# Kernel tuning notes

Hardware: AMD Instinct MI355X
Metric: run time of the kernel (lower is better)

Reference implementation:

```python
import jax, jax.numpy as jnp
import numpy as np


def setup_inputs() -> dict:
    key = jax.random.key(0)
    k1, k2, k3 = jax.random.split(key, 3)
    B, Cin, Cout, K, H, W = 4, 64, 64, 3, 160, 160
    inputs = jax.random.normal(k1, (B, Cin, H, W), dtype=jnp.float32)
    # fractional dilation rates in [1, 3]
    rate_map = 1.0 + 2.0 * jax.random.uniform(k2, (B, 1, H, W), dtype=jnp.float32)
    # xavier-uniform-ish init
    limit = float(np.sqrt(6.0 / (Cin * K * K + Cout * K * K)))
    weight = jax.random.uniform(k3, (Cout, Cin, K, K), dtype=jnp.float32,
                                minval=-limit, maxval=limit)
    bias = jnp.zeros((Cout,), dtype=jnp.float32)
    return {"inputs": inputs, "weight": weight, "rate_map": rate_map,
            "bias": bias, "stride_h": 1, "stride_w": 1}


def _pdconv2d(inputs, weight, rate_map, bias, stride_h, stride_w):
    """Perspective (fractional, per-pixel) dilated conv with same padding.

    For each output pixel, the KxK taps are placed at center + offset*rate,
    where rate comes from rate_map and may be fractional -> bilinear sampling
    with zeros outside the image.
    """
    B, C, H, W = inputs.shape
    O, _, K, _ = weight.shape
    HO = (H + stride_h - 1) // stride_h
    WO = (W + stride_w - 1) // stride_w

    rate = rate_map[:, 0, ::stride_h, ::stride_w]  # [B,HO,WO]
    cy = (jnp.arange(HO) * stride_h).astype(jnp.float32)
    cx = (jnp.arange(WO) * stride_w).astype(jnp.float32)
    off = jnp.arange(K, dtype=jnp.float32) - (K - 1) / 2.0  # centered taps

    # sampling coords [B,HO,WO,K,K]
    sy = cy[None, :, None, None, None] + off[None, None, None, :, None] * rate[:, :, :, None, None]
    sx = cx[None, None, :, None, None] + off[None, None, None, None, :] * rate[:, :, :, None, None]
    sy = jnp.broadcast_to(sy, (B, HO, WO, K, K))
    sx = jnpp = jnp.broadcast_to(sx, (B, HO, WO, K, K))
    sx = jnp_p = sx  # no-op alias (keeps names clear)

    y0 = jnp.floor(sy)
    x0 = jnp.floor(sx)
    wy = sy - y0  # bilinear weights
    wx = sx - x0
    y0i = y0.astype(jnp.int32)
    x0i = x0.astype(jnp.int32)

    img = inputs.reshape(B, C, H * W)

    def gather(idx):  # idx [B,HO,WO,K,K] -> [B,C,HO,WO,K,K]
        return jax.vmap(lambda im, ix: jnp.take(im, ix, axis=-1))(img, idx)

    acc = jnp.zeros((B, C, HO, WO, K, K), dtype=inputs.dtype)
    corners = [(0, 0, (1 - wy) * (1 - wx)), (0, 1, (1 - wy) * wx),
               (1, 0, wy * (1 - wx)), (1, 1, wy * wx)]
    for dy, dx, cw in corners:
        yy = y0i + dy
        xx = x0i + dx
        valid = (yy >= 0) & (yy < H) & (xx >= 0) & (xx < W)
        idx = jnp.clip(yy, 0, H - 1) * W + jnp.clip(xx, 0, W - 1)
        w = (cw * valid.astype(inputs.dtype))[:, None]  # [B,1,HO,WO,K,K]
        acc = acc + gather(idx) * w

    # [B,C,HO,WO,K,K] x [O,C,K,K] -> [B,O,HO,WO]
    out = jnp.einsum('bchwkl,ockl->bohw', acc, weight)
    return out + bias[None, :, None, None]


def reference(inputs, weight, rate_map, bias, stride_h, stride_w):
    return _pdconv2d(inputs, weight, rate_map, bias, stride_h, stride_w)
```

## Files before the change

kernel.cpp:

```cpp
#include <hip/hip_runtime.h>
#include <hip/hip_bf16.h>

#define NB   4
#define CIN  64
#define COUT 64
#define HH   160
#define WW   160
#define HW   (HH * WW)

#define RT   9
#define CT   39
#define RS   72
#define HIN_SHORTS (RT * CT * RS)

typedef __attribute__((ext_vector_type(8))) short bf16x8;
typedef __attribute__((ext_vector_type(4))) float f32x4;
typedef __attribute__((ext_vector_type(2))) float f32x2;
typedef __attribute__((ext_vector_type(4))) unsigned int u32x4;

static __device__ __forceinline__ short f2bf(float v) {
    return __builtin_bit_cast(short, __float2bfloat16(v));
}

__global__ void wtf_kernel(const float* __restrict__ w, short* __restrict__ wtf) {
    int i = blockIdx.x * 256 + threadIdx.x;
    if (i < 36864) {
        const int j  = i & 7;
        const int l  = (i >> 3) & 63;
        const int mt = (i >> 9) & 3;
        const int ks = (i >> 11) & 1;
        const int t  = i >> 12;
        const int o  = 16 * mt + (l & 15);
        const int c  = 32 * ks + 8 * (l >> 4) + j;
        wtf[i] = f2bf(w[(o * CIN + c) * 9 + t]);
    }
}

__global__ __launch_bounds__(256) void tin_kernel(const float* __restrict__ in,
                                                  short* __restrict__ tin) {
    const int cpx = gridDim.x >> 3;
    const int wb  = (blockIdx.x & 7) * cpx + (blockIdx.x >> 3);
    const int gid = wb * 256 + threadIdx.x;
    if (gid >= NB * HW) return;
    const int b  = gid / HW;
    const int hw = gid - b * HW;
    const float* src = in + (size_t)b * CIN * HW + hw;
    short* dst = tin + (size_t)gid * CIN;
#pragma unroll
    for (int chunk = 0; chunk < 4; ++chunk) {
        union { u32x4 v; short s[8]; } p0, p1;
#pragma unroll
        for (int cc = 0; cc < 8; ++cc)
            p0.s[cc] = f2bf(src[(size_t)(chunk * 16 + cc) * HW]);
#pragma unroll
        for (int cc = 0; cc < 8; ++cc)
            p1.s[cc] = f2bf(src[(size_t)(chunk * 16 + 8 + cc) * HW]);
        *(u32x4*)(dst + chunk * 16)     = p0.v;
        *(u32x4*)(dst + chunk * 16 + 8) = p1.v;
    }
}

static __device__ __forceinline__ void consume_tap(
    const u32x4 v00, const u32x4 v01, const u32x4 v10, const u32x4 v11,
    const float c00, const float c01, const float c10, const float c11,
    const bf16x8 wf0, const bf16x8 wf1, const bf16x8 wf2, const bf16x8 wf3,
    f32x4 acc[4])
{
    union { bf16x8 v; unsigned u[4]; } pf;
#pragma unroll
    for (int wd = 0; wd < 4; ++wd) {
        f32x2 s;
        {
            const unsigned u0 = v00[wd];
            const f32x2 xv = { __builtin_bit_cast(float, u0 << 16),
                               __builtin_bit_cast(float, u0 & 0xffff0000u) };
            s = c00 * xv;
        }
        {
            const unsigned u0 = v01[wd];
            const f32x2 xv = { __builtin_bit_cast(float, u0 << 16),
                               __builtin_bit_cast(float, u0 & 0xffff0000u) };
            s += c01 * xv;
        }
        {
            const unsigned u0 = v10[wd];
            const f32x2 xv = { __builtin_bit_cast(float, u0 << 16),
                               __builtin_bit_cast(float, u0 & 0xffff0000u) };
            s += c10 * xv;
        }
        {
            const unsigned u0 = v11[wd];
            const f32x2 xv = { __builtin_bit_cast(float, u0 << 16),
                               __builtin_bit_cast(float, u0 & 0xffff0000u) };
            s += c11 * xv;
        }
        unsigned r;
        asm("v_cvt_pk_bf16_f32 %0, %1, %2" : "=v"(r) : "v"(s.x), "v"(s.y));
        pf.u[wd] = r;
    }
    acc[0] = __builtin_amdgcn_mfma_f32_16x16x32_bf16(wf0, pf.v, acc[0], 0, 0, 0);
    acc[1] = __builtin_amdgcn_mfma_f32_16x16x32_bf16(wf1, pf.v, acc[1], 0, 0, 0);
    acc[2] = __builtin_amdgcn_mfma_f32_16x16x32_bf16(wf2, pf.v, acc[2], 0, 0, 0);
    acc[3] = __builtin_amdgcn_mfma_f32_16x16x32_bf16(wf3, pf.v, acc[3], 0, 0, 0);
}

__global__ __launch_bounds__(256, 2) void pdconv_halo_kernel(
    const short* __restrict__ tin,
    const short* __restrict__ wtf,
    const float* __restrict__ rate_map,
    const float* __restrict__ bias,
    float* __restrict__ out)
{
    __shared__ short hin[HIN_SHORTS];

    const int tid  = threadIdx.x;
    const int wave = tid >> 6;
    const int lane = tid & 63;
    const int px   = lane & 15;
    const int g    = lane >> 4;

    const int cpx = gridDim.x >> 3;
    const int bid = (blockIdx.x & 7) * cpx + (blockIdx.x >> 3);

    const int b   = bid / 400;
    const int rem = bid - b * 400;
    const int rr  = rem / 5;
    const int cc  = rem - rr * 5;
    const int oy  = 2 * rr - 3;
    const int ox  = 32 * cc - 3;

    const short* ib = tin + (size_t)b * HW * CIN;
#pragma unroll
    for (int it = 0; it < 11; ++it) {
        const int idx = it * 256 + tid;
        if (idx < RT * CT * 8) {
            const int rec = idx >> 3;
            const int cp  = idx & 7;
            const int ty  = rec / CT;
            const int tx  = rec - ty * CT;
            const int gy  = min(max(oy + ty, 0), HH - 1);
            const int gx  = min(max(ox + tx, 0), WW - 1);
            const u32x4 v = *(const u32x4*)(ib + ((size_t)gy * WW + gx) * CIN + cp * 8);
            *(u32x4*)(hin + rec * RS + cp * 8) = v;
        }
    }
    __syncthreads();

    const int row = 2 * rr + (wave >> 1);
    const int col0 = 32 * cc + 16 * (wave & 1);
    const int x   = col0 + px;
    const float rate = rate_map[b * HW + row * WW + x];
    const float fy = (float)row, fx = (float)x;

    const short* wtb = wtf + lane * 8;

    f32x4 acc[4];
#pragma unroll
    for (int mt = 0; mt < 4; ++mt) acc[mt] = (f32x4){0.f, 0.f, 0.f, 0.f};

#pragma unroll 1
    for (int t = 0; t < 9; ++t) {
        const int ky = t / 3;
        const int kx = t - 3 * ky;

        const float sy  = fy + (float)(ky - 1) * rate;
        const float sx  = fx + (float)(kx - 1) * rate;
        const float y0f = floorf(sy), x0f = floorf(sx);
        const float wy  = sy - y0f,   wx  = sx - x0f;
        const int   y0  = (int)y0f,   x0i = (int)x0f;
        const int   y1  = y0 + 1,     x1  = x0i + 1;

        const float omwy = 1.0f - wy, omwx = 1.0f - wx;
        const float vy0 = (y0 >= 0 && y0 < HH) ? 1.0f : 0.0f;
        const float vy1 = (y1 >= 0 && y1 < HH) ? 1.0f : 0.0f;
        const float vx0 = (x0i >= 0 && x0i < WW) ? 1.0f : 0.0f;
        const float vx1 = (x1 >= 0 && x1 < WW) ? 1.0f : 0.0f;

        const float c00 = omwy * omwx * vy0 * vx0;
        const float c01 = omwy * wx   * vy0 * vx1;
        const float c10 = wy   * omwx * vy1 * vx0;
        const float c11 = wy   * wx   * vy1 * vx1;

        const int rec00 = (y0 - oy) * CT + (x0i - ox);
        const short* h00 = hin + rec00 * RS + 8 * g;

        u32x4 v00[2], v01[2], v10[2], v11[2];
#pragma unroll
        for (int ks = 0; ks < 2; ++ks) {
            const short* hk = h00 + 32 * ks;
            v00[ks] = *(const u32x4*)(hk);
            v01[ks] = *(const u32x4*)(hk + RS);
            v10[ks] = *(const u32x4*)(hk + CT * RS);
            v11[ks] = *(const u32x4*)(hk + (CT + 1) * RS);
        }

#pragma unroll
        for (int ks = 0; ks < 2; ++ks) {
            const short* wb = wtb + (size_t)((t * 2 + ks) * 4) * 512;
            const bf16x8 wf0 = *(const bf16x8*)(wb);
            const bf16x8 wf1 = *(const bf16x8*)(wb + 512);
            const bf16x8 wf2 = *(const bf16x8*)(wb + 1024);
            const bf16x8 wf3 = *(const bf16x8*)(wb + 1536);
            consume_tap(v00[ks], v01[ks], v10[ks], v11[ks],
                        c00, c01, c10, c11, wf0, wf1, wf2, wf3, acc);
        }
    }

    float* op = out + (size_t)b * COUT * HW + row * WW + col0 + px;
#pragma unroll
    for (int mt = 0; mt < 4; ++mt) {
        const f32x4 bv = *(const f32x4*)(bias + 16 * mt + 4 * g);
#pragma unroll
        for (int r = 0; r < 4; ++r) {
            const int o = 16 * mt + 4 * g + r;
            op[(size_t)o * HW] = acc[mt][r] + bv[r];
        }
    }
}

__global__ void wt2_kernel(const float* __restrict__ w, short* __restrict__ wt2) {
    int i = blockIdx.x * 256 + threadIdx.x;
    if (i < 9 * COUT * CIN) {
        int c = i & 63, o = (i >> 6) & 63, t = i >> 12;
        wt2[i] = f2bf(w[(o * CIN + c) * 9 + t]);
    }
}

__global__ __launch_bounds__(256) void pdconv_mfma_kernel(
    const float* __restrict__ in, const short* __restrict__ wt2,
    const float* __restrict__ rate_map, const float* __restrict__ bias,
    float* __restrict__ out)
{
    const int tid = threadIdx.x, wave = tid >> 6, lane = tid & 63;
    const int px = lane & 15, g = lane >> 4;
    const int cpx = gridDim.x >> 3;
    const int bid = (blockIdx.x & 7) * cpx + (blockIdx.x >> 3);
    const int base = bid * 64 + wave * 16;
    const int b = base / HW, pix0 = base - b * HW;
    const int y = pix0 / WW, x0 = pix0 - y * WW, x = x0 + px;
    const float rate = rate_map[base + px];
    const float fy = (float)y, fx = (float)x;
    f32x4 acc[4];
#pragma unroll
    for (int mt = 0; mt < 4; ++mt) acc[mt] = (f32x4){0.f, 0.f, 0.f, 0.f};
    const float* img  = in + (size_t)b * CIN * HW;
    const float* imgg = img + (size_t)g * 8 * HW;
#pragma unroll 1
    for (int t = 0; t < 9; ++t) {
        const int ky = t / 3, kx = t - 3 * ky;
        const float sy = fy + (float)(ky - 1) * rate;
        const float sx = fx + (float)(kx - 1) * rate;
        const float y0f = floorf(sy), x0f = floorf(sx);
        const float wy = sy - y0f, wx = sx - x0f;
        const int y0 = (int)y0f, x0i = (int)x0f, y1 = y0 + 1, x1 = x0i + 1;
        const float omwy = 1.0f - wy, omwx = 1.0f - wx;
        const float vy0 = (y0 >= 0 && y0 < HH) ? 1.0f : 0.0f;
        const float vy1 = (y1 >= 0 && y1 < HH) ? 1.0f : 0.0f;
        const float vx0 = (x0i >= 0 && x0i < WW) ? 1.0f : 0.0f;
        const float vx1 = (x1 >= 0 && x1 < WW) ? 1.0f : 0.0f;
        const float c00 = omwy * omwx * vy0 * vx0, c01 = omwy * wx * vy0 * vx1;
        const float c10 = wy * omwx * vy1 * vx0,  c11 = wy * wx * vy1 * vx1;
        const int cy0 = min(max(y0, 0), HH - 1), cy1 = min(max(y1, 0), HH - 1);
        const int cx0 = min(max(x0i, 0), WW - 1), cx1 = min(max(x1, 0), WW - 1);
        const int i00 = cy0 * WW + cx0, i01 = cy0 * WW + cx1;
        const int i10 = cy1 * WW + cx0, i11 = cy1 * WW + cx1;
#pragma unroll
        for (int ks = 0; ks < 2; ++ks) {
            bf16x8 wf[4];
#pragma unroll
            for (int mt = 0; mt < 4; ++mt)
                wf[mt] = *(const bf16x8*)(wt2 +
                          ((t * COUT + 16 * mt + px) * CIN + 32 * ks + 8 * g));
            float a[8];
#pragma unroll
            for (int j = 0; j < 8; ++j) {
                const float* ch = imgg + (size_t)(32 * ks + j) * HW;
                a[j] = c00 * ch[i00] + c01 * ch[i01] + c10 * ch[i10] + c11 * ch[i11];
            }
            union { bf16x8 v; short s[8]; } pf;
#pragma unroll
            for (int j = 0; j < 8; ++j) pf.s[j] = f2bf(a[j]);
#pragma unroll
            for (int mt = 0; mt < 4; ++mt)
                acc[mt] = __builtin_amdgcn_mfma_f32_16x16x32_bf16(
                              wf[mt], pf.v, acc[mt], 0, 0, 0);
        }
    }
    float* op = out + (size_t)b * COUT * HW + pix0 + px;
#pragma unroll
    for (int mt = 0; mt < 4; ++mt)
#pragma unroll
        for (int r = 0; r < 4; ++r) {
            const int o = 16 * mt + 4 * g + r;
            op[(size_t)o * HW] = acc[mt][r] + bias[o];
        }
}

extern "C" void kernel_launch(void* const* d_in, const int* in_sizes, int n_in,
                              void* d_out, int out_size, void* d_ws, size_t ws_size,
                              hipStream_t stream) {
    (void)in_sizes; (void)n_in; (void)out_size;
    const float* in   = (const float*)d_in[0];
    const float* w    = (const float*)d_in[1];
    const float* rm   = (const float*)d_in[2];
    const float* bias = (const float*)d_in[3];
    float* out = (float*)d_out;

    const size_t WTF_BYTES = 36864 * sizeof(short);
    const size_t TIN_BYTES = (size_t)NB * HW * CIN * sizeof(short);

    if (ws_size >= WTF_BYTES + TIN_BYTES) {
        short* wtf = (short*)d_ws;
        short* tin = (short*)((char*)d_ws + WTF_BYTES);
        hipLaunchKernelGGL(wtf_kernel, dim3(144), dim3(256), 0, stream, w, wtf);
        hipLaunchKernelGGL(tin_kernel, dim3((NB * HW) / 256), dim3(256),
                           0, stream, in, tin);
        const int nblocks = NB * 80 * 5;
        hipLaunchKernelGGL(pdconv_halo_kernel, dim3(nblocks), dim3(256), 0,
                           stream, tin, wtf, rm, bias, out);
    } else {
        short* wt2 = (short*)d_ws;
        hipLaunchKernelGGL(wt2_kernel, dim3(144), dim3(256), 0, stream, w, wt2);
        hipLaunchKernelGGL(pdconv_mfma_kernel, dim3((NB * HW) / 64), dim3(256),
                           0, stream, in, wt2, rm, bias, out);
    }
}
```

Baseline: 49.32 us.

## Software-pipeline LDS tap loads one tap ahead and raise occupancy hint

```diff
diff --git a/kernel.cpp b/kernel.cpp
--- a/kernel.cpp
+++ b/kernel.cpp
@@ -104,7 +104,7 @@
     acc[3] = __builtin_amdgcn_mfma_f32_16x16x32_bf16(wf3, pf.v, acc[3], 0, 0, 0);
 }
 
-__global__ __launch_bounds__(256, 2) void pdconv_halo_kernel(
+__global__ __launch_bounds__(256, 3) void pdconv_halo_kernel(
     const short* __restrict__ tin,
     const short* __restrict__ wtf,
     const float* __restrict__ rate_map,
@@ -144,11 +144,10 @@
             *(u32x4*)(hin + rec * RS + cp * 8) = v;
         }
     }
-    __syncthreads();
-
-    const int row = 2 * rr + (wave >> 1);
+
+    const int row  = 2 * rr + (wave >> 1);
     const int col0 = 32 * cc + 16 * (wave & 1);
-    const int x   = col0 + px;
+    const int x    = col0 + px;
     const float rate = rate_map[b * HW + row * WW + x];
     const float fy = (float)row, fx = (float)x;
 
@@ -158,42 +157,48 @@
 #pragma unroll
     for (int mt = 0; mt < 4; ++mt) acc[mt] = (f32x4){0.f, 0.f, 0.f, 0.f};
 
-#pragma unroll 1
+    u32x4 vi00[2][2], vi01[2][2], vi10[2][2], vi11[2][2];
+    float cf[2][4];
+
+#define GEOMH(T, SL, H0) do {                                                \
+    const int gky = (T) / 3, gkx = (T) - 3 * gky;                            \
+    const float gsy = fy + (float)(gky - 1) * rate;                          \
+    const float gsx = fx + (float)(gkx - 1) * rate;                          \
+    const float gy0f = floorf(gsy), gx0f = floorf(gsx);                      \
+    const float gwy = gsy - gy0f, gwx = gsx - gx0f;                          \
+    const int gy0 = (int)gy0f, gx0 = (int)gx0f;                              \
+    const float gomwy = 1.0f - gwy, gomwx = 1.0f - gwx;                      \
+    const float gvy0 = (gy0 >= 0 && gy0 < HH) ? 1.0f : 0.0f;                 \
+    const float gvy1 = (gy0 + 1 >= 0 && gy0 + 1 < HH) ? 1.0f : 0.0f;         \
+    const float gvx0 = (gx0 >= 0 && gx0 < WW) ? 1.0f : 0.0f;                 \
+    const float gvx1 = (gx0 + 1 >= 0 && gx0 + 1 < WW) ? 1.0f : 0.0f;         \
+    cf[SL][0] = gomwy * gomwx * gvy0 * gvx0;                                 \
+    cf[SL][1] = gomwy * gwx   * gvy0 * gvx1;                                 \
+    cf[SL][2] = gwy   * gomwx * gvy1 * gvx0;                                 \
+    cf[SL][3] = gwy   * gwx   * gvy1 * gvx1;                                 \
+    H0 = hin + ((gy0 - oy) * CT + (gx0 - ox)) * RS + 8 * g;                  \
+} while (0)
+
+#define LOADIN(T, SL) do {                                                   \
+    const short* h00;                                                        \
+    GEOMH(T, SL, h00);                                                       \
+    _Pragma("unroll")                                                        \
+    for (int ks = 0; ks < 2; ++ks) {                                         \
+        const short* hk = h00 + 32 * ks;                                     \
+        vi00[SL][ks] = *(const u32x4*)(hk);                                  \
+        vi01[SL][ks] = *(const u32x4*)(hk + RS);                             \
+        vi10[SL][ks] = *(const u32x4*)(hk + CT * RS);                        \
+        vi11[SL][ks] = *(const u32x4*)(hk + (CT + 1) * RS);                  \
+    }                                                                        \
+} while (0)
+
+    __syncthreads();
+    LOADIN(0, 0);
+
+#pragma unroll
     for (int t = 0; t < 9; ++t) {
-        const int ky = t / 3;
-        const int kx = t - 3 * ky;
-
-        const float sy  = fy + (float)(ky - 1) * rate;
-        const float sx  = fx + (float)(kx - 1) * rate;
-        const float y0f = floorf(sy), x0f = floorf(sx);
-        const float wy  = sy - y0f,   wx  = sx - x0f;
-        const int   y0  = (int)y0f,   x0i = (int)x0f;
-        const int   y1  = y0 + 1,     x1  = x0i + 1;
-
-        const float omwy = 1.0f - wy, omwx = 1.0f - wx;
-        const float vy0 = (y0 >= 0 && y0 < HH) ? 1.0f : 0.0f;
-        const float vy1 = (y1 >= 0 && y1 < HH) ? 1.0f : 0.0f;
-        const float vx0 = (x0i >= 0 && x0i < WW) ? 1.0f : 0.0f;
-        const float vx1 = (x1 >= 0 && x1 < WW) ? 1.0f : 0.0f;
-
-        const float c00 = omwy * omwx * vy0 * vx0;
-        const float c01 = omwy * wx   * vy0 * vx1;
-        const float c10 = wy   * omwx * vy1 * vx0;
-        const float c11 = wy   * wx   * vy1 * vx1;
-
-        const int rec00 = (y0 - oy) * CT + (x0i - ox);
-        const short* h00 = hin + rec00 * RS + 8 * g;
-
-        u32x4 v00[2], v01[2], v10[2], v11[2];
-#pragma unroll
-        for (int ks = 0; ks < 2; ++ks) {
-            const short* hk = h00 + 32 * ks;
-            v00[ks] = *(const u32x4*)(hk);
-            v01[ks] = *(const u32x4*)(hk + RS);
-            v10[ks] = *(const u32x4*)(hk + CT * RS);
-            v11[ks] = *(const u32x4*)(hk + (CT + 1) * RS);
-        }
-
+        const int s = t & 1;
+        if (t < 8) LOADIN(t + 1, (t + 1) & 1);
 #pragma unroll
         for (int ks = 0; ks < 2; ++ks) {
             const short* wb = wtb + (size_t)((t * 2 + ks) * 4) * 512;
@@ -201,10 +206,13 @@
             const bf16x8 wf1 = *(const bf16x8*)(wb + 512);
             const bf16x8 wf2 = *(const bf16x8*)(wb + 1024);
             const bf16x8 wf3 = *(const bf16x8*)(wb + 1536);
-            consume_tap(v00[ks], v01[ks], v10[ks], v11[ks],
-                        c00, c01, c10, c11, wf0, wf1, wf2, wf3, acc);
-        }
-    }
+            consume_tap(vi00[s][ks], vi01[s][ks], vi10[s][ks], vi11[s][ks],
+                        cf[s][0], cf[s][1], cf[s][2], cf[s][3],
+                        wf0, wf1, wf2, wf3, acc);
+        }
+    }
+#undef LOADIN
+#undef GEOMH
 
     float* op = out + (size_t)b * COUT * HW + row * WW + col0 + px;
 #pragma unroll
```

New measurement: 46.78 us. 1.05x faster.
